# Kernel optimization log

Hardware: AMD Instinct MI355X
Metric: run time of the kernel (lower is better)

## Reference

```python
import jax, jax.numpy as jnp
import numpy as np

B, T, C = 4, 2048, 1024
H = 16
HD = C // H  # 64


def setup_inputs() -> dict:
    key = jax.random.key(0)
    ks = jax.random.split(key, 5)
    s = 0.02
    return {
        "x": jax.random.normal(ks[0], (B, T, C), jnp.float32),
        "qkv_w": jax.random.normal(ks[1], (3 * C, C), jnp.float32) * s,
        "qkv_b": jax.random.normal(ks[2], (3 * C,), jnp.float32) * s,
        "out_w": jax.random.normal(ks[3], (C, C), jnp.float32) * s,
        "out_b": jax.random.normal(ks[4], (C,), jnp.float32) * s,
    }


def reference(x, qkv_w, qkv_b, out_w, out_b):
    b, t, c = x.shape
    # qkv projection (torch Linear: x @ W^T + b)
    qkv = x @ qkv_w.T + qkv_b                      # (b, t, 3c)
    q, k, v = jnp.split(qkv, 3, axis=-1)
    def rsh(a):
        return a.reshape(b, t, H, HD).transpose(0, 2, 1, 3)  # (b, h, t, hd)
    q, k, v = rsh(q), rsh(k), rsh(v)
    scale = 1.0 / jnp.sqrt(jnp.float32(HD))
    attn = jnp.einsum('bhqd,bhkd->bhqk', q, k) * scale       # (b, h, t, t)
    causal = jnp.tril(jnp.ones((t, t), dtype=bool))
    attn = jnp.where(causal[None, None], attn, -jnp.inf)
    attn = jax.nn.softmax(attn, axis=-1)
    out = jnp.einsum('bhqk,bhkd->bhqd', attn, v)             # (b, h, t, hd)
    out = out.transpose(0, 2, 1, 3).reshape(b, t, c)
    return out @ out_w.T + out_b
```

## Files before the change

kernel.cpp:

```cpp
#include <hip/hip_runtime.h>

typedef __bf16 bf16x8 __attribute__((ext_vector_type(8)));
typedef __bf16 bf16x4 __attribute__((ext_vector_type(4)));
typedef float f32x4 __attribute__((ext_vector_type(4)));

typedef const __attribute__((address_space(1))) void* gptr_t;
typedef __attribute__((address_space(3))) void* lptr_t;

__device__ __forceinline__ f32x4 mfma16(bf16x8 a, bf16x8 b, f32x4 c) {
  return __builtin_amdgcn_mfma_f32_16x16x32_bf16(a, b, c, 0, 0, 0);
}

__device__ __forceinline__ void load_lds16(const __bf16* g, __bf16* l) {
  __builtin_amdgcn_global_load_lds((gptr_t)g, (lptr_t)l, 16, 0, 0);
}

__device__ __forceinline__ float fast_exp2(float x) {
#if __has_builtin(__builtin_amdgcn_exp2f)
  return __builtin_amdgcn_exp2f(x);
#else
  return exp2f(x);
#endif
}

__device__ __forceinline__ unsigned pack_bf16(float f0, float f1) {
  unsigned u0 = __builtin_bit_cast(unsigned, f0) + 0x8000u;
  unsigned u1 = __builtin_bit_cast(unsigned, f1) + 0x8000u;
  return __builtin_amdgcn_perm(u1, u0, 0x07060302);
}

__global__ __launch_bounds__(256) void convert3(
    const float* __restrict__ x, const float* __restrict__ w1,
    const float* __restrict__ w2, __bf16* __restrict__ xb,
    __bf16* __restrict__ w1b, __bf16* __restrict__ w2b) {
  int bid = blockIdx.x;
  const float* src;
  __bf16* dst;
  int base;
  if (bid < 4096) {
    src = x; dst = xb; base = bid;
  } else if (bid < 5632) {
    src = w1; dst = w1b; base = bid - 4096;
  } else {
    src = w2; dst = w2b; base = bid - 5632;
  }
  size_t off = (size_t)base * 2048 + threadIdx.x * 8;
  float4 v0 = *(const float4*)(src + off);
  float4 v1 = *(const float4*)(src + off + 4);
  bf16x8 o = {(__bf16)v0.x, (__bf16)v0.y, (__bf16)v0.z, (__bf16)v0.w,
              (__bf16)v1.x, (__bf16)v1.y, (__bf16)v1.z, (__bf16)v1.w};
  *(bf16x8*)(dst + off) = o;
}

template <bool C_BF16>
__global__ __launch_bounds__(256) void gemm_bt(
    const __bf16* __restrict__ A, const __bf16* __restrict__ B,
    const float* __restrict__ bias, void* __restrict__ Cv, int M, int N,
    int K, int qcols) {
  __shared__ __bf16 As[2][128 * 32];
  __shared__ __bf16 Bs[2][128 * 32];

  const int tid = threadIdx.x;
  const int wid = tid >> 6;
  const int lane = tid & 63;
  const int l15 = lane & 15;
  const int quad = lane >> 4;
  const int bm = blockIdx.y * 128;
  const int bn = blockIdx.x * 128;
  const int wm = (wid & 1) * 64;
  const int wn = (wid >> 1) * 64;

  const int srow = wid * 16 + (lane >> 2);
  const int schunk = ((lane & 3) ^ ((lane >> 3) & 3)) * 8;
  const __bf16* gA = A + (size_t)(bm + srow) * K + schunk;
  const __bf16* gB = B + (size_t)(bn + srow) * K + schunk;
  const int ldsoff = wid * 16 * 32;

  const int fsl = (quad ^ ((l15 >> 1) & 3)) * 8;

  f32x4 acc[4][4] = {};

  load_lds16(gA, &As[0][ldsoff]);
  load_lds16(gA + (size_t)64 * K, &As[0][64 * 32 + ldsoff]);
  load_lds16(gB, &Bs[0][ldsoff]);
  load_lds16(gB + (size_t)64 * K, &Bs[0][64 * 32 + ldsoff]);

  const int niter = K >> 5;
  for (int it = 0; it < niter; ++it) {
    const int cur = it & 1;
    __syncthreads();
    if (it + 1 < niter) {
      int k0 = (it + 1) << 5;
      load_lds16(gA + k0, &As[1 - cur][ldsoff]);
      load_lds16(gA + k0 + (size_t)64 * K, &As[1 - cur][64 * 32 + ldsoff]);
      load_lds16(gB + k0, &Bs[1 - cur][ldsoff]);
      load_lds16(gB + k0 + (size_t)64 * K, &Bs[1 - cur][64 * 32 + ldsoff]);
    }
    bf16x8 af[4], bf[4];
#pragma unroll
    for (int i = 0; i < 4; ++i)
      af[i] = *(const bf16x8*)(&As[cur][(wm + i * 16 + l15) * 32 + fsl]);
#pragma unroll
    for (int i = 0; i < 4; ++i)
      bf[i] = *(const bf16x8*)(&Bs[cur][(wn + i * 16 + l15) * 32 + fsl]);
#pragma unroll
    for (int mt = 0; mt < 4; ++mt)
#pragma unroll
      for (int nt = 0; nt < 4; ++nt)
        acc[mt][nt] = mfma16(af[mt], bf[nt], acc[mt][nt]);
  }

  const float sc = (bn < qcols) ? 0.18033688011112043f : 1.0f;
#pragma unroll
  for (int mt = 0; mt < 4; ++mt) {
#pragma unroll
    for (int nt = 0; nt < 4; ++nt) {
      int gc = bn + wn + nt * 16 + l15;
      float bv = bias[gc];
#pragma unroll
      for (int r = 0; r < 4; ++r) {
        int gr = bm + wm + mt * 16 + quad * 4 + r;
        float val = (acc[mt][nt][r] + bv) * sc;
        if constexpr (C_BF16)
          ((__bf16*)Cv)[(size_t)gr * N + gc] = (__bf16)val;
        else
          ((float*)Cv)[(size_t)gr * N + gc] = val;
      }
    }
  }
}

template <bool MASK>
__device__ __forceinline__ void softmax_block(f32x4 (&s)[2][4],
                                              float (&lsum)[2][4],
                                              __bf16* __restrict__ psw,
                                              int kv0, int qrow_base, int quad,
                                              int l15) {
#pragma unroll
  for (int mt = 0; mt < 2; ++mt) {
#pragma unroll
    for (int r = 0; r < 4; ++r) {
      int prow = mt * 16 + quad * 4 + r;
      float p[4];
#pragma unroll
      for (int nt = 0; nt < 4; ++nt) {
        p[nt] = fast_exp2(s[mt][nt][r]);
        if constexpr (MASK) {
          if ((kv0 + nt * 16 + l15) > (qrow_base + prow)) p[nt] = 0.f;
        }
      }
      lsum[mt][r] += (p[0] + p[1]) + (p[2] + p[3]);
      uint2 w = {pack_bf16(p[0], p[1]), pack_bf16(p[2], p[3])};
      int o = ((l15 >> 1) ^ (prow & 7)) & 7;
      *(uint2*)(psw + prow * 64 + o * 8 + 4 * (l15 & 1)) = w;
    }
  }
}

__global__ __launch_bounds__(256) void attn_kernel(
    const __bf16* __restrict__ qkv, __bf16* __restrict__ out) {
  constexpr int T = 2048, C3 = 3072;
  constexpr int KVSTEP = 64 * C3;
  __shared__ __bf16 Ks[2][64 * 64];
  __shared__ __bf16 Vt[2][64 * 64];
  __shared__ __bf16 Ps[4][32 * 64];

  const int tid = threadIdx.x;
  const int wid = tid >> 6;
  const int lane = tid & 63;
  const int l15 = lane & 15;
  const int quad = lane >> 4;
  const int bh = blockIdx.x;
  const int pb = blockIdx.y;
  const int b = bh >> 4, h = bh & 15;
  const size_t rowbase = (size_t)b * T;

  const int kr = tid >> 3;
  const int kc = tid & 7;
  const int vj = tid >> 4;
  const int vn = tid & 15;

  const __bf16* gk_base = qkv + rowbase * C3 + 1024 + h * 64 + kr * C3 + kc * 8;
  const __bf16* gv_base = qkv + rowbase * C3 + 2048 + h * 64 + vj * C3 + vn * 4;

  int ks_st0 = kr * 64 + ((kc ^ (kr & 7)) * 8);
  int ks_st1 = (kr + 32) * 64 + ((kc ^ ((kr + 32) & 7)) * 8);
  int vt_st[4];
#pragma unroll
  for (int dd = 0; dd < 4; ++dd) {
    int d = 4 * vn + dd;
    vt_st[dd] = d * 64 + ((((vj >> 1) ^ (d & 7) ^ (d >> 3)) & 7) * 8) +
                4 * (vj & 1);
  }
  int kf_off[4][2];
#pragma unroll
  for (int nt = 0; nt < 4; ++nt)
#pragma unroll
    for (int ksi = 0; ksi < 2; ++ksi)
      kf_off[nt][ksi] =
          (nt * 16 + l15) * 64 + (((4 * ksi + quad) ^ (l15 & 7)) * 8);
  int pf_off[2][2];
#pragma unroll
  for (int mt = 0; mt < 2; ++mt)
#pragma unroll
    for (int ksi = 0; ksi < 2; ++ksi)
      pf_off[mt][ksi] =
          (mt * 16 + l15) * 64 + (((4 * ksi + quad) ^ (l15 & 7)) * 8);
  int vf_off[4][2];
#pragma unroll
  for (int ntv = 0; ntv < 4; ++ntv)
#pragma unroll
    for (int ksi = 0; ksi < 2; ++ksi) {
      int d = ntv * 16 + l15;
      vf_off[ntv][ksi] =
          d * 64 + ((((4 * ksi + quad) ^ (d & 7) ^ (d >> 3)) & 7) * 8);
    }

#pragma unroll 1
  for (int phase = 0; phase < 2; ++phase) {
    const int qp = phase == 0 ? pb : 15 - pb;
    const int q0 = qp * 128;
    const int ntiles = 2 * qp + 2;
    const int qrow_base = q0 + wid * 32;

    bf16x8 qf[2][2];
#pragma unroll
    for (int mt = 0; mt < 2; ++mt)
#pragma unroll
      for (int ksi = 0; ksi < 2; ++ksi)
        qf[mt][ksi] = *(const bf16x8*)(
            qkv + (rowbase + qrow_base + mt * 16 + l15) * C3 + h * 64 +
            ksi * 32 + quad * 8);

    f32x4 acc[2][4] = {};
    float lsum[2][4] = {};

    const __bf16* gk = gk_base;
    const __bf16* gv = gv_base;

    bf16x8 kreg[2];
    bf16x4 vreg[4];
    kreg[0] = *(const bf16x8*)(gk);
    kreg[1] = *(const bf16x8*)(gk + 32 * C3);
#pragma unroll
    for (int i = 0; i < 4; ++i)
      vreg[i] = *(const bf16x4*)(gv + i * 16 * C3);

    __syncthreads();

    for (int j = 0; j < ntiles; ++j) {
      __bf16* ksb = Ks[j & 1];
      __bf16* vtb = Vt[j & 1];
      *(bf16x8*)(ksb + ks_st0) = kreg[0];
      *(bf16x8*)(ksb + ks_st1) = kreg[1];
#pragma unroll
      for (int dd = 0; dd < 4; ++dd) {
        bf16x4 t = {vreg[0][dd], vreg[1][dd], vreg[2][dd], vreg[3][dd]};
        *(bf16x4*)(vtb + vt_st[dd]) = t;
      }
      if (j + 1 < ntiles) {
        gk += KVSTEP;
        gv += KVSTEP;
        kreg[0] = *(const bf16x8*)(gk);
        kreg[1] = *(const bf16x8*)(gk + 32 * C3);
#pragma unroll
        for (int i = 0; i < 4; ++i)
          vreg[i] = *(const bf16x4*)(gv + i * 16 * C3);
      }
      __syncthreads();

      const int kv0 = j * 64;
      f32x4 s[2][4] = {};
#pragma unroll
      for (int nt = 0; nt < 4; ++nt) {
#pragma unroll
        for (int ksi = 0; ksi < 2; ++ksi) {
          bf16x8 kf = *(const bf16x8*)(ksb + kf_off[nt][ksi]);
#pragma unroll
          for (int mt = 0; mt < 2; ++mt)
            s[mt][nt] = mfma16(qf[mt][ksi], kf, s[mt][nt]);
        }
      }
      if ((kv0 + 63) > qrow_base)
        softmax_block<true>(s, lsum, Ps[wid], kv0, qrow_base, quad, l15);
      else
        softmax_block<false>(s, lsum, Ps[wid], kv0, qrow_base, quad, l15);

#pragma unroll
      for (int ksi = 0; ksi < 2; ++ksi) {
        bf16x8 pf[2];
#pragma unroll
        for (int mt = 0; mt < 2; ++mt)
          pf[mt] = *(const bf16x8*)(Ps[wid] + pf_off[mt][ksi]);
#pragma unroll
        for (int ntv = 0; ntv < 4; ++ntv) {
          bf16x8 vf = *(const bf16x8*)(vtb + vf_off[ntv][ksi]);
#pragma unroll
          for (int mt = 0; mt < 2; ++mt)
            acc[mt][ntv] = mfma16(pf[mt], vf, acc[mt][ntv]);
        }
      }
    }

#pragma unroll
    for (int mt = 0; mt < 2; ++mt)
#pragma unroll
      for (int r = 0; r < 4; ++r) {
        float l = lsum[mt][r];
        l += __shfl_xor(l, 1);
        l += __shfl_xor(l, 2);
        l += __shfl_xor(l, 4);
        l += __shfl_xor(l, 8);
        float inv = 1.0f / l;
        int row = qrow_base + mt * 16 + quad * 4 + r;
        size_t ob = (rowbase + row) * 1024 + h * 64;
#pragma unroll
        for (int ntv = 0; ntv < 4; ++ntv)
          out[ob + ntv * 16 + l15] = (__bf16)(acc[mt][ntv][r] * inv);
      }
  }
}

extern "C" void kernel_launch(void* const* d_in, const int* in_sizes, int n_in,
                              void* d_out, int out_size, void* d_ws,
                              size_t ws_size, hipStream_t stream) {
  const float* x = (const float*)d_in[0];
  const float* qkv_w = (const float*)d_in[1];
  const float* qkv_b = (const float*)d_in[2];
  const float* out_w = (const float*)d_in[3];
  const float* out_b = (const float*)d_in[4];
  float* out = (float*)d_out;

  __bf16* qkv_ws = (__bf16*)d_ws;
  __bf16* attn_ws = qkv_ws + (size_t)8192 * 3072;
  __bf16* xb = attn_ws + (size_t)8192 * 1024;
  __bf16* wqb = xb + (size_t)8192 * 1024;
  __bf16* wob = wqb + (size_t)3072 * 1024;

  convert3<<<6144, 256, 0, stream>>>(x, qkv_w, out_w, xb, wqb, wob);
  gemm_bt<true><<<dim3(24, 64), 256, 0, stream>>>(xb, wqb, qkv_b, qkv_ws,
                                                  8192, 3072, 1024, 1024);
  attn_kernel<<<dim3(64, 8), 256, 0, stream>>>(qkv_ws, attn_ws);
  gemm_bt<false><<<dim3(8, 64), 256, 0, stream>>>(attn_ws, wob, out_b, out,
                                                  8192, 1024, 1024, 0);
}
```

Baseline: 243.3 us.

## Rewrite GEMM as 256x128 tile, 512 threads, 4-stage LDS pipeline

```diff
diff --git a/kernel.cpp b/kernel.cpp
--- a/kernel.cpp
+++ b/kernel.cpp
@@ -53,61 +53,89 @@
 }
 
 template <bool C_BF16>
-__global__ __launch_bounds__(256) void gemm_bt(
+__global__ __launch_bounds__(512) void gemm256(
     const __bf16* __restrict__ A, const __bf16* __restrict__ B,
-    const float* __restrict__ bias, void* __restrict__ Cv, int M, int N,
-    int K, int qcols) {
-  __shared__ __bf16 As[2][128 * 32];
-  __shared__ __bf16 Bs[2][128 * 32];
+    const float* __restrict__ bias, void* __restrict__ Cv, int N, int K,
+    int qcols) {
+  __shared__ __bf16 As[4][256 * 32];
+  __shared__ __bf16 Bs[4][128 * 32];
 
   const int tid = threadIdx.x;
   const int wid = tid >> 6;
   const int lane = tid & 63;
   const int l15 = lane & 15;
   const int quad = lane >> 4;
-  const int bm = blockIdx.y * 128;
-  const int bn = blockIdx.x * 128;
-  const int wm = (wid & 1) * 64;
-  const int wn = (wid >> 1) * 64;
-
-  const int srow = wid * 16 + (lane >> 2);
-  const int schunk = ((lane & 3) ^ ((lane >> 3) & 3)) * 8;
+  const int wr = wid >> 1;
+  const int wc = wid & 1;
+
+  const int nwg = gridDim.x * gridDim.y;
+  int id = blockIdx.y * gridDim.x + blockIdx.x;
+  id = (id & 7) * (nwg >> 3) + (id >> 3);
+  const int bn = (id % gridDim.x) * 128;
+  const int bm = (id / gridDim.x) * 256;
+
+  const int srow = tid >> 2;
+  const int schunk = ((tid & 3) ^ ((tid >> 3) & 3)) * 8;
   const __bf16* gA = A + (size_t)(bm + srow) * K + schunk;
   const __bf16* gB = B + (size_t)(bn + srow) * K + schunk;
-  const int ldsoff = wid * 16 * 32;
+  const int a_st0 = wid * 512;
+  const int a_st1 = 4096 + wid * 512;
+  const int b_st = wid * 512;
 
   const int fsl = (quad ^ ((l15 >> 1) & 3)) * 8;
+  int af_off[4], bf_off[4];
+#pragma unroll
+  for (int mt = 0; mt < 4; ++mt)
+    af_off[mt] = (wr * 64 + mt * 16 + l15) * 32 + fsl;
+#pragma unroll
+  for (int nt = 0; nt < 4; ++nt)
+    bf_off[nt] = (wc * 64 + nt * 16 + l15) * 32 + fsl;
 
   f32x4 acc[4][4] = {};
 
-  load_lds16(gA, &As[0][ldsoff]);
-  load_lds16(gA + (size_t)64 * K, &As[0][64 * 32 + ldsoff]);
-  load_lds16(gB, &Bs[0][ldsoff]);
-  load_lds16(gB + (size_t)64 * K, &Bs[0][64 * 32 + ldsoff]);
-
-  const int niter = K >> 5;
-  for (int it = 0; it < niter; ++it) {
-    const int cur = it & 1;
-    __syncthreads();
-    if (it + 1 < niter) {
-      int k0 = (it + 1) << 5;
-      load_lds16(gA + k0, &As[1 - cur][ldsoff]);
-      load_lds16(gA + k0 + (size_t)64 * K, &As[1 - cur][64 * 32 + ldsoff]);
-      load_lds16(gB + k0, &Bs[1 - cur][ldsoff]);
-      load_lds16(gB + k0 + (size_t)64 * K, &Bs[1 - cur][64 * 32 + ldsoff]);
-    }
+  load_lds16(gA, &As[0][a_st0]);
+  load_lds16(gA + (size_t)128 * K, &As[0][a_st1]);
+  load_lds16(gB, &Bs[0][b_st]);
+  load_lds16(gA + 32, &As[1][a_st0]);
+  load_lds16(gA + 32 + (size_t)128 * K, &As[1][a_st1]);
+  load_lds16(gB + 32, &Bs[1][b_st]);
+  asm volatile("s_waitcnt vmcnt(3)" ::: "memory");
+  __builtin_amdgcn_s_barrier();
+
+  const int ntt = K >> 5;
+  for (int j = 0; j < ntt; ++j) {
+    const __bf16* ab = As[j & 3];
+    const __bf16* bb = Bs[j & 3];
     bf16x8 af[4], bf[4];
 #pragma unroll
-    for (int i = 0; i < 4; ++i)
-      af[i] = *(const bf16x8*)(&As[cur][(wm + i * 16 + l15) * 32 + fsl]);
-#pragma unroll
-    for (int i = 0; i < 4; ++i)
-      bf[i] = *(const bf16x8*)(&Bs[cur][(wn + i * 16 + l15) * 32 + fsl]);
+    for (int mt = 0; mt < 4; ++mt)
+      af[mt] = *(const bf16x8*)(ab + af_off[mt]);
+#pragma unroll
+    for (int nt = 0; nt < 4; ++nt)
+      bf[nt] = *(const bf16x8*)(bb + bf_off[nt]);
+    const bool more = (j + 2 < ntt);
+    if (more) {
+      const int sb = (j + 2) & 3;
+      const size_t koff = (size_t)(j + 2) << 5;
+      load_lds16(gA + koff, &As[sb][a_st0]);
+      load_lds16(gA + koff + (size_t)128 * K, &As[sb][a_st1]);
+      load_lds16(gB + koff, &Bs[sb][b_st]);
+    }
+    __builtin_amdgcn_s_barrier();
+    asm volatile("s_waitcnt lgkmcnt(0)" ::: "memory");
+    __builtin_amdgcn_sched_barrier(0);
+    __builtin_amdgcn_s_setprio(1);
 #pragma unroll
     for (int mt = 0; mt < 4; ++mt)
 #pragma unroll
       for (int nt = 0; nt < 4; ++nt)
         acc[mt][nt] = mfma16(af[mt], bf[nt], acc[mt][nt]);
+    __builtin_amdgcn_s_setprio(0);
+    if (more)
+      asm volatile("s_waitcnt vmcnt(3)" ::: "memory");
+    else
+      asm volatile("s_waitcnt vmcnt(0)" ::: "memory");
+    __builtin_amdgcn_s_barrier();
   }
 
   const float sc = (bn < qcols) ? 0.18033688011112043f : 1.0f;
@@ -115,11 +143,11 @@
   for (int mt = 0; mt < 4; ++mt) {
 #pragma unroll
     for (int nt = 0; nt < 4; ++nt) {
-      int gc = bn + wn + nt * 16 + l15;
+      int gc = bn + wc * 64 + nt * 16 + l15;
       float bv = bias[gc];
 #pragma unroll
       for (int r = 0; r < 4; ++r) {
-        int gr = bm + wm + mt * 16 + quad * 4 + r;
+        int gr = bm + wr * 64 + mt * 16 + quad * 4 + r;
         float val = (acc[mt][nt][r] + bv) * sc;
         if constexpr (C_BF16)
           ((__bf16*)Cv)[(size_t)gr * N + gc] = (__bf16)val;
@@ -338,9 +366,9 @@
   __bf16* wob = wqb + (size_t)3072 * 1024;
 
   convert3<<<6144, 256, 0, stream>>>(x, qkv_w, out_w, xb, wqb, wob);
-  gemm_bt<true><<<dim3(24, 64), 256, 0, stream>>>(xb, wqb, qkv_b, qkv_ws,
-                                                  8192, 3072, 1024, 1024);
+  gemm256<true><<<dim3(24, 32), 512, 0, stream>>>(xb, wqb, qkv_b, qkv_ws,
+                                                  3072, 1024, 1024);
   attn_kernel<<<dim3(64, 8), 256, 0, stream>>>(qkv_ws, attn_ws);
-  gemm_bt<false><<<dim3(8, 64), 256, 0, stream>>>(attn_ws, wob, out_b, out,
-                                                  8192, 1024, 1024, 0);
-}
+  gemm256<false><<<dim3(8, 32), 512, 0, stream>>>(attn_ws, wob, out_b, out,
+                                                  1024, 1024, 0);
+}
```

Measured after the change: 247.7 us. Within noise of the previous version (+1.8%).

## Use 256x256-tile 8-wave pipelined GEMM for QKV projection

Applied to the files above, without the earlier changes.

```diff
diff --git a/kernel.cpp b/kernel.cpp
--- a/kernel.cpp
+++ b/kernel.cpp
@@ -53,6 +53,138 @@
 }
 
 template <bool C_BF16>
+__global__ __launch_bounds__(512, 2) void gemm256p(
+    const __bf16* __restrict__ A, const __bf16* __restrict__ B,
+    const float* __restrict__ bias, void* __restrict__ Cv, int N, int K,
+    int qcols) {
+  __shared__ __bf16 As[2 * 2 * 128 * 64];
+  __shared__ __bf16 Bs[2 * 2 * 128 * 64];
+
+  const int tid = threadIdx.x;
+  const int wid = tid >> 6;
+  const int lane = tid & 63;
+  const int l15 = lane & 15;
+  const int quad = lane >> 4;
+  const int wr = wid >> 2;
+  const int wc = wid & 3;
+
+  const int bn = blockIdx.x * 256;
+  const int bm = blockIdx.y * 256;
+
+  const int srow = tid >> 3;
+  const int soct = ((tid & 7) ^ (srow & 7)) * 8;
+  const __bf16* gA = A + (size_t)(bm + srow) * K + soct;
+  const __bf16* gB = B + (size_t)(bn + srow) * K + soct;
+  __bf16* lA = As + tid * 8;
+  __bf16* lB = Bs + tid * 8;
+
+#define STAGE_A(h, g, ko, slot)                             \
+  load_lds16(gA + (size_t)((h)*128 + (g)*64) * K + (ko),    \
+             lA + (slot)*16384 + (h)*8192 + (g)*4096)
+#define STAGE_B(h, g, ko, slot)                             \
+  load_lds16(gB + (size_t)((h)*128 + (g)*64) * K + (ko),    \
+             lB + (slot)*16384 + (h)*8192 + (g)*4096)
+
+  int fo[2];
+#pragma unroll
+  for (int ksi = 0; ksi < 2; ++ksi)
+    fo[ksi] = l15 * 64 + (((4 * ksi + quad) ^ (l15 & 7)) * 8);
+
+  f32x4 acc[8][4] = {};
+
+  STAGE_A(0, 0, 0, 0); STAGE_A(0, 1, 0, 0);
+  STAGE_A(1, 0, 0, 0); STAGE_A(1, 1, 0, 0);
+  STAGE_B(0, 0, 0, 0); STAGE_B(0, 1, 0, 0);
+  STAGE_B(1, 0, 0, 0); STAGE_B(1, 1, 0, 0);
+  STAGE_B(0, 0, 64, 1); STAGE_B(0, 1, 64, 1);
+  STAGE_B(1, 0, 64, 1); STAGE_B(1, 1, 64, 1);
+  asm volatile("s_waitcnt vmcnt(4)" ::: "memory");
+  asm volatile("s_barrier" ::: "memory");
+
+  const int nit = K >> 7;
+#pragma unroll 1
+  for (int i = 0; i < nit; ++i) {
+    const bool more = (i + 1 < nit);
+    const int ko1 = (2 * i + 1) << 6;
+    const int ko2 = (2 * i + 2) << 6;
+    const int ko3 = (2 * i + 3) << 6;
+    bf16x8 bfr[4][2];
+#pragma unroll
+    for (int ts = 0; ts < 2; ++ts) {
+#pragma unroll
+      for (int q = 0; q < 4; ++q) {
+        bf16x8 af[2][2];
+#pragma unroll
+        for (int j = 0; j < 2; ++j)
+#pragma unroll
+          for (int ksi = 0; ksi < 2; ++ksi)
+            af[j][ksi] = *(const bf16x8*)(As + ts * 16384 + wr * 8192 +
+                                          (2 * q + j) * 1024 + fo[ksi]);
+        if (q == 0) {
+#pragma unroll
+          for (int nt = 0; nt < 4; ++nt)
+#pragma unroll
+            for (int ksi = 0; ksi < 2; ++ksi)
+              bfr[nt][ksi] =
+                  *(const bf16x8*)(Bs + ts * 16384 + (wc >> 1) * 8192 +
+                                   (wc & 1) * 4096 + nt * 1024 + fo[ksi]);
+        }
+        if (ts == 0) {
+          if (q == 0)      { STAGE_A(0, 0, ko1, 1); STAGE_A(0, 1, ko1, 1); }
+          else if (q == 1) { STAGE_A(1, 0, ko1, 1); STAGE_A(1, 1, ko1, 1); }
+          else if (q == 2) { if (more) { STAGE_B(0, 0, ko2, 0); STAGE_B(0, 1, ko2, 0); } }
+          else             { if (more) { STAGE_B(1, 0, ko2, 0); STAGE_B(1, 1, ko2, 0); } }
+        } else {
+          if (q == 0)      { if (more) { STAGE_A(0, 0, ko2, 0); STAGE_A(0, 1, ko2, 0); } }
+          else if (q == 1) { if (more) { STAGE_A(1, 0, ko2, 0); STAGE_A(1, 1, ko2, 0); } }
+          else if (q == 2) { if (more) { STAGE_B(0, 0, ko3, 1); STAGE_B(0, 1, ko3, 1); } }
+          else             { if (more) { STAGE_B(1, 0, ko3, 1); STAGE_B(1, 1, ko3, 1); } }
+        }
+        asm volatile("s_barrier" ::: "memory");
+        asm volatile("s_waitcnt lgkmcnt(0)" ::: "memory");
+        __builtin_amdgcn_sched_barrier(0);
+        __builtin_amdgcn_s_setprio(1);
+#pragma unroll
+        for (int ksi = 0; ksi < 2; ++ksi)
+#pragma unroll
+          for (int nt = 0; nt < 4; ++nt)
+#pragma unroll
+            for (int j = 0; j < 2; ++j)
+              acc[2 * q + j][nt] =
+                  mfma16(af[j][ksi], bfr[nt][ksi], acc[2 * q + j][nt]);
+        __builtin_amdgcn_s_setprio(0);
+        if (q == 3) {
+          if (more) asm volatile("s_waitcnt vmcnt(4)" ::: "memory");
+          else      asm volatile("s_waitcnt vmcnt(0)" ::: "memory");
+        }
+        asm volatile("s_barrier" ::: "memory");
+      }
+    }
+  }
+#undef STAGE_A
+#undef STAGE_B
+
+  const float sc = (bn < qcols) ? 0.18033688011112043f : 1.0f;
+#pragma unroll
+  for (int mt = 0; mt < 8; ++mt) {
+#pragma unroll
+    for (int nt = 0; nt < 4; ++nt) {
+      int gc = bn + wc * 64 + nt * 16 + l15;
+      float bv = bias[gc];
+#pragma unroll
+      for (int r = 0; r < 4; ++r) {
+        int gr = bm + wr * 128 + mt * 16 + quad * 4 + r;
+        float val = (acc[mt][nt][r] + bv) * sc;
+        if constexpr (C_BF16)
+          ((__bf16*)Cv)[(size_t)gr * N + gc] = (__bf16)val;
+        else
+          ((float*)Cv)[(size_t)gr * N + gc] = val;
+      }
+    }
+  }
+}
+
+template <bool C_BF16>
 __global__ __launch_bounds__(256) void gemm_bt(
     const __bf16* __restrict__ A, const __bf16* __restrict__ B,
     const float* __restrict__ bias, void* __restrict__ Cv, int M, int N,
@@ -338,8 +470,8 @@
   __bf16* wob = wqb + (size_t)3072 * 1024;
 
   convert3<<<6144, 256, 0, stream>>>(x, qkv_w, out_w, xb, wqb, wob);
-  gemm_bt<true><<<dim3(24, 64), 256, 0, stream>>>(xb, wqb, qkv_b, qkv_ws,
-                                                  8192, 3072, 1024, 1024);
+  gemm256p<true><<<dim3(12, 32), 512, 0, stream>>>(xb, wqb, qkv_b, qkv_ws,
+                                                   3072, 1024, 1024);
   attn_kernel<<<dim3(64, 8), 256, 0, stream>>>(qkv_ws, attn_ws);
   gemm_bt<false><<<dim3(8, 64), 256, 0, stream>>>(attn_ws, wob, out_b, out,
                                                   8192, 1024, 1024, 0);
```

Result: slower. 251.5 us (+3.3%).

## Software-pipeline attention KV tiles two deep with priority hints and packed output stores

Applied to the files above, without the earlier changes.

```diff
diff --git a/kernel.cpp b/kernel.cpp
--- a/kernel.cpp
+++ b/kernel.cpp
@@ -216,6 +216,58 @@
           d * 64 + ((((4 * ksi + quad) ^ (d & 7) ^ (d >> 3)) & 7) * 8);
     }
 
+#define KV_TILE(J, BUF, WK, WV, LK, LV)                                       \
+  {                                                                           \
+    const int kv0 = (J) * 64;                                                 \
+    __bf16* ksb = Ks[BUF];                                                    \
+    __bf16* vtb = Vt[BUF];                                                    \
+    f32x4 s[2][4] = {};                                                       \
+    __builtin_amdgcn_s_setprio(1);                                            \
+    _Pragma("unroll") for (int nt = 0; nt < 4; ++nt) {                        \
+      _Pragma("unroll") for (int ksi = 0; ksi < 2; ++ksi) {                   \
+        bf16x8 kf = *(const bf16x8*)(ksb + kf_off[nt][ksi]);                  \
+        _Pragma("unroll") for (int mt = 0; mt < 2; ++mt) s[mt][nt] =          \
+            mfma16(qf[mt][ksi], kf, s[mt][nt]);                               \
+      }                                                                       \
+    }                                                                         \
+    __builtin_amdgcn_s_setprio(0);                                            \
+    if ((J) + 1 < ntiles) {                 \
+      __bf16* ksn = Ks[1 - (BUF)];                                            \
+      __bf16* vtn = Vt[1 - (BUF)];                                            \
+      *(bf16x8*)(ksn + ks_st0) = WK[0];                                       \
+      *(bf16x8*)(ksn + ks_st1) = WK[1];                                       \
+      _Pragma("unroll") for (int dd = 0; dd < 4; ++dd) {                      \
+        bf16x4 t = {WV[0][dd], WV[1][dd], WV[2][dd], WV[3][dd]};              \
+        *(bf16x4*)(vtn + vt_st[dd]) = t;                                      \
+      }                                                                       \
+    }                                                                         \
+    if ((J) + 2 < ntiles) {                  \
+      const __bf16* gnk = gk_base + (size_t)((J) + 2) * KVSTEP;               \
+      const __bf16* gnv = gv_base + (size_t)((J) + 2) * KVSTEP;               \
+      LK[0] = *(const bf16x8*)(gnk);                                          \
+      LK[1] = *(const bf16x8*)(gnk + 32 * C3);                                \
+      _Pragma("unroll") for (int i = 0; i < 4; ++i) LV[i] =                   \
+          *(const bf16x4*)(gnv + (size_t)i * 16 * C3);                        \
+    }                                                                         \
+    if ((kv0 + 63) > qrow_base)                                               \
+      softmax_block<true>(s, lsum, Ps[wid], kv0, qrow_base, quad, l15);       \
+    else                                                                      \
+      softmax_block<false>(s, lsum, Ps[wid], kv0, qrow_base, quad, l15);      \
+    __builtin_amdgcn_s_setprio(1);                                            \
+    _Pragma("unroll") for (int ksi = 0; ksi < 2; ++ksi) {                     \
+      bf16x8 pf[2];                                                           \
+      _Pragma("unroll") for (int mt = 0; mt < 2; ++mt) pf[mt] =               \
+          *(const bf16x8*)(Ps[wid] + pf_off[mt][ksi]);                        \
+      _Pragma("unroll") for (int ntv = 0; ntv < 4; ++ntv) {                   \
+        bf16x8 vf = *(const bf16x8*)(vtb + vf_off[ntv][ksi]);                 \
+        _Pragma("unroll") for (int mt = 0; mt < 2; ++mt) acc[mt][ntv] =       \
+            mfma16(pf[mt], vf, acc[mt][ntv]);                                 \
+      }                                                                       \
+    }                                                                         \
+    __builtin_amdgcn_s_setprio(0);                                            \
+    __syncthreads();                                                          \
+  }
+
 #pragma unroll 1
   for (int phase = 0; phase < 2; ++phase) {
     const int qp = phase == 0 ? pb : 15 - pb;
@@ -235,73 +287,36 @@
     f32x4 acc[2][4] = {};
     float lsum[2][4] = {};
 
-    const __bf16* gk = gk_base;
-    const __bf16* gv = gv_base;
-
-    bf16x8 kreg[2];
-    bf16x4 vreg[4];
-    kreg[0] = *(const bf16x8*)(gk);
-    kreg[1] = *(const bf16x8*)(gk + 32 * C3);
+    bf16x8 kA[2], kB[2];
+    bf16x4 vA[4], vB[4];
+    kA[0] = *(const bf16x8*)(gk_base);
+    kA[1] = *(const bf16x8*)(gk_base + 32 * C3);
 #pragma unroll
     for (int i = 0; i < 4; ++i)
-      vreg[i] = *(const bf16x4*)(gv + i * 16 * C3);
+      vA[i] = *(const bf16x4*)(gv_base + (size_t)i * 16 * C3);
+    kB[0] = *(const bf16x8*)(gk_base + KVSTEP);
+    kB[1] = *(const bf16x8*)(gk_base + KVSTEP + 32 * C3);
+#pragma unroll
+    for (int i = 0; i < 4; ++i)
+      vB[i] = *(const bf16x4*)(gv_base + KVSTEP + (size_t)i * 16 * C3);
 
     __syncthreads();
 
-    for (int j = 0; j < ntiles; ++j) {
-      __bf16* ksb = Ks[j & 1];
-      __bf16* vtb = Vt[j & 1];
-      *(bf16x8*)(ksb + ks_st0) = kreg[0];
-      *(bf16x8*)(ksb + ks_st1) = kreg[1];
-#pragma unroll
-      for (int dd = 0; dd < 4; ++dd) {
-        bf16x4 t = {vreg[0][dd], vreg[1][dd], vreg[2][dd], vreg[3][dd]};
-        *(bf16x4*)(vtb + vt_st[dd]) = t;
-      }
-      if (j + 1 < ntiles) {
-        gk += KVSTEP;
-        gv += KVSTEP;
-        kreg[0] = *(const bf16x8*)(gk);
-        kreg[1] = *(const bf16x8*)(gk + 32 * C3);
-#pragma unroll
-        for (int i = 0; i < 4; ++i)
-          vreg[i] = *(const bf16x4*)(gv + i * 16 * C3);
-      }
-      __syncthreads();
-
-      const int kv0 = j * 64;
-      f32x4 s[2][4] = {};
-#pragma unroll
-      for (int nt = 0; nt < 4; ++nt) {
-#pragma unroll
-        for (int ksi = 0; ksi < 2; ++ksi) {
-          bf16x8 kf = *(const bf16x8*)(ksb + kf_off[nt][ksi]);
-#pragma unroll
-          for (int mt = 0; mt < 2; ++mt)
-            s[mt][nt] = mfma16(qf[mt][ksi], kf, s[mt][nt]);
-        }
-      }
-      if ((kv0 + 63) > qrow_base)
-        softmax_block<true>(s, lsum, Ps[wid], kv0, qrow_base, quad, l15);
-      else
-        softmax_block<false>(s, lsum, Ps[wid], kv0, qrow_base, quad, l15);
-
-#pragma unroll
-      for (int ksi = 0; ksi < 2; ++ksi) {
-        bf16x8 pf[2];
-#pragma unroll
-        for (int mt = 0; mt < 2; ++mt)
-          pf[mt] = *(const bf16x8*)(Ps[wid] + pf_off[mt][ksi]);
-#pragma unroll
-        for (int ntv = 0; ntv < 4; ++ntv) {
-          bf16x8 vf = *(const bf16x8*)(vtb + vf_off[ntv][ksi]);
-#pragma unroll
-          for (int mt = 0; mt < 2; ++mt)
-            acc[mt][ntv] = mfma16(pf[mt], vf, acc[mt][ntv]);
-        }
-      }
-    }
-
+    *(bf16x8*)(Ks[0] + ks_st0) = kA[0];
+    *(bf16x8*)(Ks[0] + ks_st1) = kA[1];
+#pragma unroll
+    for (int dd = 0; dd < 4; ++dd) {
+      bf16x4 t = {vA[0][dd], vA[1][dd], vA[2][dd], vA[3][dd]};
+      *(bf16x4*)(Vt[0] + vt_st[dd]) = t;
+    }
+    __syncthreads();
+
+    for (int jj = 0; jj < ntiles; jj += 2) {
+      KV_TILE(jj, 0, kB, vB, kA, vA);
+      KV_TILE(jj + 1, 1, kA, vA, kB, vB);
+    }
+
+    const int srcl = (lane & 48) + ((2 * l15) & 15);
 #pragma unroll
     for (int mt = 0; mt < 2; ++mt)
 #pragma unroll
@@ -315,10 +330,20 @@
         int row = qrow_base + mt * 16 + quad * 4 + r;
         size_t ob = (rowbase + row) * 1024 + h * 64;
 #pragma unroll
-        for (int ntv = 0; ntv < 4; ++ntv)
-          out[ob + ntv * 16 + l15] = (__bf16)(acc[mt][ntv][r] * inv);
+        for (int np = 0; np < 2; ++np) {
+          float a0 = acc[mt][2 * np][r] * inv;
+          float a1 = acc[mt][2 * np + 1][r] * inv;
+          float t0 = __shfl(a0, srcl);
+          float t1 = __shfl(a1, srcl);
+          float u0 = __shfl(a0, srcl + 1);
+          float u1 = __shfl(a1, srcl + 1);
+          float lo = (l15 < 8) ? t0 : t1;
+          float hi = (l15 < 8) ? u0 : u1;
+          *(unsigned*)(out + ob + np * 32 + 2 * l15) = pack_bf16(lo, hi);
+        }
       }
   }
+#undef KV_TILE
 }
 
 extern "C" void kernel_launch(void* const* d_in, const int* in_sizes, int n_in,
```

Measured after the change: 273.3 us. 1.12x slower.
